# Kernel tuning notes

Hardware: AMD Instinct MI355X
Metric: run time of the kernel (lower is better)

The kernel has to match this reference:

```python
import jax, jax.numpy as jnp
import numpy as np
from jax import lax


def _lstm_layer(x, W_ih, W_hh, b_ih, b_hh):
    """Single LSTM layer, batch_first x: [B, T, in] -> (out [B,T,H], h_n [B,H], c_n [B,H]).
    PyTorch gate order: i, f, g, o."""
    B, T, _ = x.shape
    H = W_hh.shape[1]
    # Precompute input contributions for all timesteps (one big GEMM).
    xg = jnp.einsum('bti,gi->btg', x, W_ih) + b_ih + b_hh  # [B, T, 4H]
    h0 = jnp.zeros((B, H), dtype=x.dtype)
    c0 = jnp.zeros((B, H), dtype=x.dtype)

    def step(carry, g_t):
        h, c = carry
        gates = g_t + h @ W_hh.T  # [B, 4H]
        i, f, g, o = jnp.split(gates, 4, axis=-1)
        i = jax.nn.sigmoid(i)
        f = jax.nn.sigmoid(f)
        g = jnp.tanh(g)
        o = jax.nn.sigmoid(o)
        c = f * c + i * g
        h = o * jnp.tanh(c)
        return (h, c), h

    (h_n, c_n), hs = lax.scan(step, (h0, c0), jnp.swapaxes(xg, 0, 1))  # hs: [T, B, H]
    return jnp.swapaxes(hs, 0, 1), h_n, c_n


def setup_inputs() -> dict:
    key = jax.random.key(0)
    ks = jax.random.split(key, 12)
    H = 128
    IN = 1
    B, T = 256, 2048
    s = 1.0 / np.sqrt(H)  # PyTorch default init scale

    def u(k, shape):
        return jax.random.uniform(k, shape, jnp.float32, -s, s)

    return {
        'x': jax.random.normal(ks[0], (B, T, IN), jnp.float32),
        'W_ih_l0': u(ks[1], (4 * H, IN)),
        'W_hh_l0': u(ks[2], (4 * H, H)),
        'b_ih_l0': u(ks[3], (4 * H,)),
        'b_hh_l0': u(ks[4], (4 * H,)),
        'W_ih_l1': u(ks[5], (4 * H, H)),
        'W_hh_l1': u(ks[6], (4 * H, H)),
        'b_ih_l1': u(ks[7], (4 * H,)),
        'b_hh_l1': u(ks[8], (4 * H,)),
        'W_fc': u(ks[9], (1, H)),
        'b_fc': u(ks[10], (1,)),
    }


def reference(x, W_ih_l0, W_hh_l0, b_ih_l0, b_hh_l0,
              W_ih_l1, W_hh_l1, b_ih_l1, b_hh_l1, W_fc, b_fc):
    out0, h0, c0 = _lstm_layer(x, W_ih_l0, W_hh_l0, b_ih_l0, b_hh_l0)
    out1, h1, c1 = _lstm_layer(out0, W_ih_l1, W_hh_l1, b_ih_l1, b_hh_l1)
    last = out1[:, -1, :]                 # [B, H]
    y = last @ W_fc.T + b_fc              # [B, 1]
    h_n = jnp.stack([h0, h1], axis=0)     # [num_layers, B, H]
    c_n = jnp.stack([c0, c1], axis=0)
    return (y, h_n, c_n)
```

## Files before the change

### kernel.cpp

```cpp
#include <hip/hip_runtime.h>

#define T_SEQ 2048
#define HDIM  128
#define GDIM  512
#define BATCH 256

typedef _Float16 f16;
typedef _Float16 f16x2 __attribute__((ext_vector_type(2)));
typedef _Float16 f16x8 __attribute__((ext_vector_type(8)));

#if __has_builtin(__builtin_amdgcn_fdot2)
__device__ __forceinline__ float dot2(f16x2 a, f16x2 b, float c) {
    return __builtin_amdgcn_fdot2(a, b, c, false);
}
#else
__device__ __forceinline__ float dot2(f16x2 a, f16x2 b, float c) {
    return c + (float)a[0] * (float)b[0] + (float)a[1] * (float)b[1];
}
#endif

__device__ __forceinline__ f16x2 mk2(float a, float b) {
    f16x2 r; r[0] = (f16)a; r[1] = (f16)b; return r;
}
__device__ __forceinline__ f16x2 pr(f16x8 v, int m) {
    f16x2 r; r[0] = v[2 * m]; r[1] = v[2 * m + 1]; return r;
}

__device__ __forceinline__ float sigm(float x) {
    return __builtin_amdgcn_rcpf(1.0f + __expf(-x));
}
__device__ __forceinline__ float tanh_fast(float x) {
    float e = __expf(2.0f * x);
    return 1.0f - 2.0f * __builtin_amdgcn_rcpf(e + 1.0f);
}

__global__ __launch_bounds__(512) __attribute__((amdgpu_waves_per_eu(2, 2)))
void lstm_fused(const float* __restrict__ x,
                const float* __restrict__ Wih0,
                const float* __restrict__ Whh0,
                const float* __restrict__ bih0,
                const float* __restrict__ bhh0,
                const float* __restrict__ Wih1,
                const float* __restrict__ Whh1,
                const float* __restrict__ bih1,
                const float* __restrict__ bhh1,
                const float* __restrict__ Wfc,
                const float* __restrict__ bfc,
                float* __restrict__ out)
{
    __shared__ __align__(16) float xs[T_SEQ];
    __shared__ __align__(16) f16   h0b[2][HDIM];
    __shared__ __align__(16) f16   h1b[2][HDIM];
    __shared__ float ysum[8];

    const int t    = threadIdx.x;
    const int b    = blockIdx.x;
    const int gate = t & 3;
    const int u    = t >> 2;
    const int row  = gate * HDIM + u;

    ((float4*)xs)[t] = ((const float4*)(x + (size_t)b * T_SEQ))[t];

    f16x2 w0[64];
    f16x2 wi[64];
    f16x2 wl[64];
    {
        const float4* p0 = (const float4*)(Whh0 + (size_t)row * HDIM);
        const float4* p1 = (const float4*)(Wih1 + (size_t)row * HDIM);
        const float4* p2 = (const float4*)(Whh1 + (size_t)row * HDIM);
#pragma unroll
        for (int c = 0; c < 32; ++c) {
            float4 v = p0[c];
            w0[2 * c] = mk2(v.x, v.y); w0[2 * c + 1] = mk2(v.z, v.w);
        }
#pragma unroll
        for (int c = 0; c < 32; ++c) {
            float4 v = p1[c];
            wi[2 * c] = mk2(v.x, v.y); wi[2 * c + 1] = mk2(v.z, v.w);
        }
#pragma unroll
        for (int c = 0; c < 32; ++c) {
            float4 v = p2[c];
            wl[2 * c] = mk2(v.x, v.y); wl[2 * c + 1] = mk2(v.z, v.w);
        }
    }
    const float wx0   = Wih0[row];
    const float bias0 = bih0[row] + bhh0[row];
    const float bias1 = bih1[row] + bhh1[row];

    if (t < HDIM) { h0b[0][t] = (f16)0.f; h1b[0][t] = (f16)0.f; }
    float c0r = 0.f, c1r = 0.f;
    float h0fin = 0.f, h1fin = 0.f;
    __syncthreads();

    const int lb = (t & 63) & ~3;

    for (int i = 0; i <= T_SEQ; ++i) {
        const int p = i & 1, q = p ^ 1;
        const f16x8* h0p = (const f16x8*)h0b[p];
        const f16x8* h1p = (const f16x8*)h1b[p];

        float a0a = (i < T_SEQ ? xs[i] : 0.f) * wx0 + bias0, a0b = 0.f;
        float a1a = bias1, a1b = 0.f;
#pragma unroll
        for (int c = 0; c < 16; c += 2) {
            f16x8 ha = h0p[c], hb = h0p[c + 1];
#pragma unroll
            for (int m = 0; m < 4; ++m) {
                a0a = dot2(w0[4 * c + m],     pr(ha, m), a0a);
                a1a = dot2(wi[4 * c + m],     pr(ha, m), a1a);
                a0b = dot2(w0[4 * c + 4 + m], pr(hb, m), a0b);
                a1b = dot2(wi[4 * c + 4 + m], pr(hb, m), a1b);
            }
        }
#pragma unroll
        for (int c = 0; c < 16; c += 2) {
            f16x8 ha = h1p[c], hb = h1p[c + 1];
#pragma unroll
            for (int m = 0; m < 4; ++m) {
                a1a = dot2(wl[4 * c + m],     pr(ha, m), a1a);
                a1b = dot2(wl[4 * c + 4 + m], pr(hb, m), a1b);
            }
        }
        const float a0 = a0a + a0b;
        const float a1 = a1a + a1b;

        float gi0 = __shfl(a0, lb + 0), gf0 = __shfl(a0, lb + 1);
        float gg0 = __shfl(a0, lb + 2), go0 = __shfl(a0, lb + 3);
        float gi1 = __shfl(a1, lb + 0), gf1 = __shfl(a1, lb + 1);
        float gg1 = __shfl(a1, lb + 2), go1 = __shfl(a1, lb + 3);

        if (i < T_SEQ) {
            c0r   = sigm(gf0) * c0r + sigm(gi0) * tanh_fast(gg0);
            h0fin = sigm(go0) * tanh_fast(c0r);
            if (gate == 0) h0b[q][u] = (f16)h0fin;
        }
        if (i >= 1) {
            c1r   = sigm(gf1) * c1r + sigm(gi1) * tanh_fast(gg1);
            h1fin = sigm(go1) * tanh_fast(c1r);
            if (gate == 0) h1b[q][u] = (f16)h1fin;
        } else if (gate == 0) {
            h1b[q][u] = (f16)0.f;
        }
        __syncthreads();
    }

    float* hn = out + BATCH;
    float* cn = out + BATCH + 2 * BATCH * HDIM;
    if (gate == 0) {
        hn[(size_t)b * HDIM + u] = h0fin;
        cn[(size_t)b * HDIM + u] = c0r;
        hn[BATCH * HDIM + (size_t)b * HDIM + u] = h1fin;
        cn[BATCH * HDIM + (size_t)b * HDIM + u] = c1r;
    }
    float part = (gate == 0) ? h1fin * Wfc[u] : 0.f;
#pragma unroll
    for (int o = 32; o >= 1; o >>= 1) part += __shfl_xor(part, o);
    if ((t & 63) == 0) ysum[t >> 6] = part;
    __syncthreads();
    if (t == 0) {
        float s = 0.f;
#pragma unroll
        for (int w = 0; w < 8; ++w) s += ysum[w];
        out[b] = s + bfc[0];
    }
}

extern "C" void kernel_launch(void* const* d_in, const int* in_sizes, int n_in,
                              void* d_out, int out_size, void* d_ws, size_t ws_size,
                              hipStream_t stream) {
    const float* x    = (const float*)d_in[0];
    const float* Wih0 = (const float*)d_in[1];
    const float* Whh0 = (const float*)d_in[2];
    const float* bih0 = (const float*)d_in[3];
    const float* bhh0 = (const float*)d_in[4];
    const float* Wih1 = (const float*)d_in[5];
    const float* Whh1 = (const float*)d_in[6];
    const float* bih1 = (const float*)d_in[7];
    const float* bhh1 = (const float*)d_in[8];
    const float* Wfc  = (const float*)d_in[9];
    const float* bfc  = (const float*)d_in[10];
    lstm_fused<<<BATCH, 512, 0, stream>>>(x, Wih0, Whh0, bih0, bhh0,
                                          Wih1, Whh1, bih1, bhh1,
                                          Wfc, bfc, (float*)d_out);
}
```

Measured before the change: 2.842 ms.

## Split each gate-row dot product across two threads with 1024-thread blocks

Doubles the block size to 1024 threads so each gate row's 128-wide recurrent dot products are split into two halves, each handled by a separate thread. The partial sums are combined with an xor shuffle. Per-thread weight registers and per-step dot-product latency are halved, shortening the serial critical path of each timestep. The cost is twice the waves per block, an extra shuffle per step, more redundant nonlinearity evaluation, and a heavier barrier each step.

```diff
diff --git a/kernel.cpp b/kernel.cpp
--- a/kernel.cpp
+++ b/kernel.cpp
@@ -2,7 +2,6 @@
 
 #define T_SEQ 2048
 #define HDIM  128
-#define GDIM  512
 #define BATCH 256
 
 typedef _Float16 f16;
@@ -34,7 +33,7 @@
     return 1.0f - 2.0f * __builtin_amdgcn_rcpf(e + 1.0f);
 }
 
-__global__ __launch_bounds__(512) __attribute__((amdgpu_waves_per_eu(2, 2)))
+__global__ __launch_bounds__(1024) __attribute__((amdgpu_waves_per_eu(4, 4)))
 void lstm_fused(const float* __restrict__ x,
                 const float* __restrict__ Wih0,
                 const float* __restrict__ Whh0,
@@ -51,35 +50,37 @@
     __shared__ __align__(16) float xs[T_SEQ];
     __shared__ __align__(16) f16   h0b[2][HDIM];
     __shared__ __align__(16) f16   h1b[2][HDIM];
-    __shared__ float ysum[8];
+    __shared__ float ysum[16];
 
     const int t    = threadIdx.x;
     const int b    = blockIdx.x;
-    const int gate = t & 3;
-    const int u    = t >> 2;
+    const int half = t & 1;
+    const int gate = (t >> 1) & 3;
+    const int u    = t >> 3;
     const int row  = gate * HDIM + u;
 
-    ((float4*)xs)[t] = ((const float4*)(x + (size_t)b * T_SEQ))[t];
+    ((float2*)xs)[t] = ((const float2*)(x + (size_t)b * T_SEQ))[t];
 
-    f16x2 w0[64];
-    f16x2 wi[64];
-    f16x2 wl[64];
+    f16x2 w0[32];
+    f16x2 wi[32];
+    f16x2 wl[32];
     {
-        const float4* p0 = (const float4*)(Whh0 + (size_t)row * HDIM);
-        const float4* p1 = (const float4*)(Wih1 + (size_t)row * HDIM);
-        const float4* p2 = (const float4*)(Whh1 + (size_t)row * HDIM);
+        const size_t off = (size_t)row * HDIM + half * 64;
+        const float4* p0 = (const float4*)(Whh0 + off);
+        const float4* p1 = (const float4*)(Wih1 + off);
+        const float4* p2 = (const float4*)(Whh1 + off);
 #pragma unroll
-        for (int c = 0; c < 32; ++c) {
+        for (int c = 0; c < 16; ++c) {
             float4 v = p0[c];
             w0[2 * c] = mk2(v.x, v.y); w0[2 * c + 1] = mk2(v.z, v.w);
         }
 #pragma unroll
-        for (int c = 0; c < 32; ++c) {
+        for (int c = 0; c < 16; ++c) {
             float4 v = p1[c];
             wi[2 * c] = mk2(v.x, v.y); wi[2 * c + 1] = mk2(v.z, v.w);
         }
 #pragma unroll
-        for (int c = 0; c < 32; ++c) {
+        for (int c = 0; c < 16; ++c) {
             float4 v = p2[c];
             wl[2 * c] = mk2(v.x, v.y); wl[2 * c + 1] = mk2(v.z, v.w);
         }
@@ -93,17 +94,18 @@
     float h0fin = 0.f, h1fin = 0.f;
     __syncthreads();
 
-    const int lb = (t & 63) & ~3;
+    const int lbase = (t & 63) & ~7;
 
     for (int i = 0; i <= T_SEQ; ++i) {
         const int p = i & 1, q = p ^ 1;
-        const f16x8* h0p = (const f16x8*)h0b[p];
-        const f16x8* h1p = (const f16x8*)h1b[p];
+        const f16x8* h0p = (const f16x8*)(h0b[p] + half * 64);
+        const f16x8* h1p = (const f16x8*)(h1b[p] + half * 64);
 
-        float a0a = (i < T_SEQ ? xs[i] : 0.f) * wx0 + bias0, a0b = 0.f;
-        float a1a = bias1, a1b = 0.f;
+        float a0a = half ? 0.f : (i < T_SEQ ? xs[i] : 0.f) * wx0 + bias0;
+        float a1a = half ? 0.f : bias1;
+        float a0b = 0.f, a1b = 0.f;
 #pragma unroll
-        for (int c = 0; c < 16; c += 2) {
+        for (int c = 0; c < 8; c += 2) {
             f16x8 ha = h0p[c], hb = h0p[c + 1];
 #pragma unroll
             for (int m = 0; m < 4; ++m) {
@@ -114,7 +116,7 @@
             }
         }
 #pragma unroll
-        for (int c = 0; c < 16; c += 2) {
+        for (int c = 0; c < 8; c += 2) {
             f16x8 ha = h1p[c], hb = h1p[c + 1];
 #pragma unroll
             for (int m = 0; m < 4; ++m) {
@@ -122,24 +124,26 @@
                 a1b = dot2(wl[4 * c + 4 + m], pr(hb, m), a1b);
             }
         }
-        const float a0 = a0a + a0b;
-        const float a1 = a1a + a1b;
+        float a0 = a0a + a0b;
+        float a1 = a1a + a1b;
+        a0 += __shfl_xor(a0, 1);
+        a1 += __shfl_xor(a1, 1);
 
-        float gi0 = __shfl(a0, lb + 0), gf0 = __shfl(a0, lb + 1);
-        float gg0 = __shfl(a0, lb + 2), go0 = __shfl(a0, lb + 3);
-        float gi1 = __shfl(a1, lb + 0), gf1 = __shfl(a1, lb + 1);
-        float gg1 = __shfl(a1, lb + 2), go1 = __shfl(a1, lb + 3);
+        float gi0 = __shfl(a0, lbase + 0), gf0 = __shfl(a0, lbase + 2);
+        float gg0 = __shfl(a0, lbase + 4), go0 = __shfl(a0, lbase + 6);
+        float gi1 = __shfl(a1, lbase + 0), gf1 = __shfl(a1, lbase + 2);
+        float gg1 = __shfl(a1, lbase + 4), go1 = __shfl(a1, lbase + 6);
 
         if (i < T_SEQ) {
             c0r   = sigm(gf0) * c0r + sigm(gi0) * tanh_fast(gg0);
             h0fin = sigm(go0) * tanh_fast(c0r);
-            if (gate == 0) h0b[q][u] = (f16)h0fin;
+            if ((t & 7) == 0) h0b[q][u] = (f16)h0fin;
         }
         if (i >= 1) {
             c1r   = sigm(gf1) * c1r + sigm(gi1) * tanh_fast(gg1);
             h1fin = sigm(go1) * tanh_fast(c1r);
-            if (gate == 0) h1b[q][u] = (f16)h1fin;
-        } else if (gate == 0) {
+            if ((t & 7) == 0) h1b[q][u] = (f16)h1fin;
+        } else if ((t & 7) == 0) {
             h1b[q][u] = (f16)0.f;
         }
         __syncthreads();
@@ -147,13 +151,13 @@
 
     float* hn = out + BATCH;
     float* cn = out + BATCH + 2 * BATCH * HDIM;
-    if (gate == 0) {
+    if ((t & 7) == 0) {
         hn[(size_t)b * HDIM + u] = h0fin;
         cn[(size_t)b * HDIM + u] = c0r;
         hn[BATCH * HDIM + (size_t)b * HDIM + u] = h1fin;
         cn[BATCH * HDIM + (size_t)b * HDIM + u] = c1r;
     }
-    float part = (gate == 0) ? h1fin * Wfc[u] : 0.f;
+    float part = ((t & 7) == 0) ? h1fin * Wfc[u] : 0.f;
 #pragma unroll
     for (int o = 32; o >= 1; o >>= 1) part += __shfl_xor(part, o);
     if ((t & 63) == 0) ysum[t >> 6] = part;
@@ -161,7 +165,7 @@
     if (t == 0) {
         float s = 0.f;
 #pragma unroll
-        for (int w = 0; w < 8; ++w) s += ysum[w];
+        for (int w = 0; w < 16; ++w) s += ysum[w];
         out[b] = s + bfc[0];
     }
 }
@@ -180,7 +184,7 @@
     const float* bhh1 = (const float*)d_in[8];
     const float* Wfc  = (const float*)d_in[9];
     const float* bfc  = (const float*)d_in[10];
-    lstm_fused<<<BATCH, 512, 0, stream>>>(x, Wih0, Whh0, bih0, bhh0,
-                                          Wih1, Whh1, bih1, bhh1,
-                                          Wfc, bfc, (float*)d_out);
+    lstm_fused<<<BATCH, 1024, 0, stream>>>(x, Wih0, Whh0, bih0, bhh0,
+                                           Wih1, Whh1, bih1, bhh1,
+                                           Wfc, bfc, (float*)d_out);
 }
```

After: 3.544 ms. 1.25x slower.
